# Optimization experiments

Hardware: AMD Instinct MI355X
Metric: run time of the kernel (lower is better)

Reference implementation:

```python
import jax, jax.numpy as jnp
import numpy as np
import math

B, L, IN_DIM, OUT_DIM = 2, 2048, 128, 128
H, DH = 8, 32            # num_heads, dim_head
ED = H * DH * 2          # embed_dim = 512
DEPTH = 1
LAMBDA_INIT = 0.8 - 0.6 * math.exp(-0.3 * (DEPTH + 1))
EPS = 1e-8


def setup_inputs() -> dict:
    key = jax.random.key(0)
    ks = jax.random.split(key, 10)
    x = jax.random.normal(ks[0], (B, 1, L, IN_DIM), dtype=jnp.float32)
    mask_2d = jax.random.bernoulli(ks[1], 0.9, (B, L, L))
    Wq = jax.random.normal(ks[2], (IN_DIM, ED), dtype=jnp.float32) * 0.05
    Wkv = jax.random.normal(ks[3], (IN_DIM, 2 * ED), dtype=jnp.float32) * 0.05
    Wout = jax.random.normal(ks[4], (ED, OUT_DIM), dtype=jnp.float32) * 0.05
    lambda_q1 = jax.random.normal(ks[5], (DH,), dtype=jnp.float32) * 0.1
    lambda_k1 = jax.random.normal(ks[6], (DH,), dtype=jnp.float32) * 0.1
    lambda_q2 = jax.random.normal(ks[7], (DH,), dtype=jnp.float32) * 0.1
    lambda_k2 = jax.random.normal(ks[8], (DH,), dtype=jnp.float32) * 0.1
    gamma = jnp.ones((2 * DH,), dtype=jnp.float32)
    return {"x": x, "mask_2d": mask_2d, "Wq": Wq, "Wkv": Wkv, "Wout": Wout,
            "lambda_q1": lambda_q1, "lambda_k1": lambda_k1,
            "lambda_q2": lambda_q2, "lambda_k2": lambda_k2, "gamma": gamma}


def reference(x, mask_2d, Wq, Wkv, Wout, lambda_q1, lambda_k1, lambda_q2, lambda_k2, gamma):
    b = x.shape[0]
    xs = x[:, 0]                                   # [b, L, in_dim]
    q = xs @ Wq                                    # [b, L, 2*H*DH]
    k, v = jnp.split(xs @ Wkv, 2, axis=-1)
    q = q.reshape(b, L, 2 * H, DH).transpose(0, 2, 1, 3) * (DH ** -0.5)  # [b,2H,L,d]
    k = k.reshape(b, L, 2 * H, DH).transpose(0, 2, 1, 3)                 # [b,2H,L,d]
    v = v.reshape(b, L, H, 2 * DH).transpose(0, 2, 1, 3)                 # [b,H,L,2d]
    dots = jnp.einsum('bnld,bnmd->bnlm', q, k)     # [b,2H,L,L]
    mask_value = -jnp.finfo(dots.dtype).max
    dots = jnp.where(mask_2d[:, None, :, :], dots, mask_value)
    attn_w = jax.nn.softmax(dots.astype(jnp.float32), axis=-1).astype(dots.dtype)
    lam1 = jnp.exp(jnp.sum(lambda_q1 * lambda_k1))
    lam2 = jnp.exp(jnp.sum(lambda_q2 * lambda_k2))
    lam = lam1 - lam2 + LAMBDA_INIT
    attn_w = attn_w.reshape(b, H, 2, L, L)
    attn_w = attn_w[:, :, 0] - lam * attn_w[:, :, 1]   # [b,H,L,L]
    attn = jnp.einsum('bhlm,bhmd->bhld', attn_w, v)    # [b,H,L,2d]
    rms = jnp.sqrt(jnp.mean(attn ** 2, axis=-1, keepdims=True))
    attn = gamma * (attn / (rms + EPS)) * (1.0 - LAMBDA_INIT)
    out = attn.transpose(0, 2, 1, 3).reshape(b, L, H * 2 * DH) @ Wout  # [b,L,out_dim]
    return out[:, None]                             # [b,1,L,out_dim]
```

## Files before the change

### kernel.cpp

```cpp
#include <hip/hip_runtime.h>
#include <float.h>
#include <math.h>

typedef __attribute__((ext_vector_type(8))) short short8;
typedef __attribute__((ext_vector_type(4))) float f32x4;
typedef __attribute__((ext_vector_type(4))) unsigned short ushort4v;

constexpr int SEQL = 2048;
constexpr int NQH  = 16;
constexpr int NVH  = 8;
constexpr int DHD  = 32;
constexpr float LAMB_INIT = 0.4707130183436648f;
constexpr float REPS      = 1e-8f;
constexpr float QW        = 0.25503492f;

#if __has_builtin(__builtin_amdgcn_exp2f)
#define EXPW(x) __builtin_amdgcn_exp2f(x)
#else
#define EXPW(x) exp2f(x)
#endif

static __device__ __forceinline__ unsigned short f2bf(float f) {
    union { float f; unsigned u; } a; a.f = f;
    unsigned u = a.u;
    u += 0x7fffu + ((u >> 16) & 1u);
    return (unsigned short)(u >> 16);
}

static __device__ __forceinline__ unsigned cvtpk(float lo, float hi) {
    unsigned r;
    asm("v_cvt_pk_bf16_f32 %0, %1, %2" : "=v"(r) : "v"(lo), "v"(hi));
    return r;
}

static __device__ __forceinline__ void stage16(const unsigned short* g, unsigned short* l) {
    __builtin_amdgcn_global_load_lds(
        (const __attribute__((address_space(1))) unsigned int*)g,
        (__attribute__((address_space(3))) unsigned int*)l, 16, 0, 0);
}

__global__ __launch_bounds__(256) void pack_prep_kernel(
        const unsigned char* __restrict__ mb, const int* __restrict__ mi,
        unsigned long long* __restrict__ bits,
        const float* __restrict__ x, const float* __restrict__ Wq,
        const float* __restrict__ Wkv, const float* __restrict__ Wout,
        unsigned short* __restrict__ xb, unsigned short* __restrict__ Wf,
        unsigned short* __restrict__ WfO) {
    __shared__ int cnt[256];
    int t = threadIdx.x;
    int c = 0;
    #pragma unroll
    for (int i = 0; i < 16; ++i) c += (mb[t * 16 + i] != 0);
    cnt[t] = c;
    __syncthreads();
    for (int s = 128; s > 0; s >>= 1) { if (t < s) cnt[t] += cnt[t + s]; __syncthreads(); }
    int f = cnt[0] > 2048;
    int gtid = blockIdx.x * 256 + t;
    int nthr = gridDim.x * 256;
    {
        const int total = 2 * SEQL * (SEQL / 64);
        int wid = blockIdx.x * 4 + (t >> 6);
        int lane = t & 63;
        int stride = gridDim.x * 4;
        for (int w = wid; w < total; w += stride) {
            int e = w * 64 + lane;
            int v = f ? (int)mb[e] : mi[e];
            unsigned long long b = __ballot(v != 0);
            if (lane == 0) bits[w] = b;
        }
    }
    {
        float4 v = ((const float4*)x)[gtid];
        ushort4v o = { f2bf(v.x), f2bf(v.y), f2bf(v.z), f2bf(v.w) };
        ((ushort4v*)xb)[gtid] = o;
    }
    for (int e = gtid; e < 262144; e += nthr) {
        int k = e >> 11, cc = e & 2047;
        if (cc < 1536) {
            float v = (cc < 512) ? Wq[(size_t)k * 512 + cc] * QW
                                 : Wkv[(size_t)k * 1024 + (cc - 512)];
            int cp = cc >> 4, lr = cc & 15, kk = k >> 5, lg = (k >> 3) & 3, j = k & 7;
            Wf[(((size_t)(cp * 4 + kk) * 4 + lg) * 16 + lr) * 8 + j] = f2bf(v);
        }
    }
    if (gtid < 65536) {
        int k = gtid >> 7, cc = gtid & 127;
        float v = Wout[gtid];
        int cp = cc >> 4, lr = cc & 15, kk = k >> 5, lg = (k >> 3) & 3, j = k & 7;
        WfO[(((size_t)(cp * 16 + kk) * 4 + lg) * 16 + lr) * 8 + j] = f2bf(v);
    }
}

__global__ __launch_bounds__(256) void qkv_mfma_kernel(
        const unsigned short* __restrict__ xb, const unsigned short* __restrict__ Wf,
        unsigned short* __restrict__ Q, unsigned short* __restrict__ Kf,
        unsigned short* __restrict__ Vf) {
    int t = threadIdx.x, w = t >> 6, lane = t & 63, lr = lane & 15, lg = lane >> 4;
    int lid = blockIdx.x;
    int swz = (lid & 7) * 192 + (lid >> 3);
    int by = swz >> 6, bx = swz & 63;
    int r0 = bx * 64 + w * 16;
    short8 ax[4];
    #pragma unroll
    for (int kk = 0; kk < 4; ++kk)
        ax[kk] = *(const short8*)(xb + (size_t)(r0 + lr) * 128 + kk * 32 + lg * 8);
    f32x4 acc[4];
    #pragma unroll
    for (int ct = 0; ct < 4; ++ct) acc[ct] = (f32x4){0.f, 0.f, 0.f, 0.f};
    #pragma unroll
    for (int ct = 0; ct < 4; ++ct) {
        int cp = by * 4 + ct;
        #pragma unroll
        for (int kk = 0; kk < 4; ++kk) {
            short8 bw = *(const short8*)(Wf + (size_t)(cp * 4 + kk) * 512 + lane * 8);
            acc[ct] = __builtin_amdgcn_mfma_f32_16x16x32_bf16(ax[kk], bw, acc[ct], 0, 0, 0);
        }
    }
    int gr0 = r0 + 4 * lg;
    int b = gr0 >> 11;
    if (by < 8) {
        #pragma unroll
        for (int ct = 0; ct < 4; ++ct) {
            int col = by * 64 + 16 * ct + lr;
            int n = col >> 5, d = col & 31;
            #pragma unroll
            for (int r = 0; r < 4; ++r) {
                int l = (gr0 + r) & 2047;
                Q[(((size_t)(b * NQH + n)) * SEQL + l) * DHD + d] = f2bf(acc[ct][r]);
            }
        }
    } else if (by < 16) {
        #pragma unroll
        for (int ct = 0; ct < 4; ++ct) {
            int ck = by * 64 + 16 * ct + lr - 512;
            int n = ck >> 5, dk = ck & 31;
            size_t hb = ((size_t)(b * NQH + n)) * 65536 + (dk >> 3) * 128 + (dk & 7);
            #pragma unroll
            for (int r = 0; r < 4; ++r) {
                int l = (gr0 + r) & 2047;
                Kf[hb + (size_t)((l >> 6) * 4 + ((l >> 4) & 3)) * 512 + (l & 15) * 8]
                    = f2bf(acc[ct][r]);
            }
        }
    } else {
        #pragma unroll
        for (int ct = 0; ct < 4; ++ct) {
            int cv = by * 64 + 16 * ct + lr - 1024;
            int h = cv >> 6, d = cv & 63;
            size_t hb = ((size_t)(b * NVH + h)) * 131072 + (d >> 4) * 512 + (d & 15) * 8;
            #pragma unroll
            for (int r = 0; r < 4; ++r) {
                int l = (gr0 + r) & 2047;
                Vf[hb + (size_t)((l >> 6) * 2 + ((l >> 5) & 1)) * 2048
                      + ((l >> 4) & 1) * 4 + ((l >> 2) & 3) * 128 + (l & 3)]
                    = f2bf(acc[ct][r]);
            }
        }
    }
}

__global__ __launch_bounds__(256, 2) void attn_kernel(
        const unsigned short* __restrict__ Q, const unsigned short* __restrict__ Kf,
        const unsigned short* __restrict__ Vf, const unsigned long long* __restrict__ bits,
        const float* __restrict__ lq1, const float* __restrict__ lk1,
        const float* __restrict__ lq2, const float* __restrict__ lk2,
        const float* __restrict__ gamma, unsigned short* __restrict__ A) {
    __shared__ unsigned short lds[4][8192];
    int tid = threadIdx.x;
    int w = tid >> 6, lane = tid & 63;
    int lr = lane & 15, lg = lane >> 4;
    int lid = blockIdx.y * 32 + blockIdx.x;
    int swz = (lid & 7) * 64 + (lid >> 3);
    int qtile = swz & 31, bh = swz >> 5;
    int b = bh >> 3, h = bh & 7;
    int q0 = qtile * 64 + w * 16;
    int bnA = b * NQH + 2 * h;

    short8 aqA = *(const short8*)(Q + (((size_t)bnA) * SEQL + q0 + lr) * DHD + lg * 8);
    short8 aqB = *(const short8*)(Q + (((size_t)(bnA + 1)) * SEQL + q0 + lr) * DHD + lg * 8);
    const unsigned short* KA = Kf + ((size_t)bnA) * 65536;
    const unsigned short* KB = KA + 65536;
    const unsigned short* VB = Vf + ((size_t)(b * NVH + h)) * 131072;
    const unsigned long long* mrow = bits + ((size_t)b * SEQL + q0 + lr) * 32;

    auto stage_tile = [&](int bf, int it) {
        #pragma unroll
        for (int j = 0; j < 4; ++j) {
            int c = 4 * w + j;
            const unsigned short* src =
                (c < 4) ? (KA + it * 2048 + c * 512)
              : (c < 8) ? (KB + it * 2048 + (c - 4) * 512)
                        : (VB + it * 4096 + (c - 8) * 512);
            stage16(src + lane * 8, &lds[bf][c * 512]);
        }
    };

    f32x4 oA[4], oB[4];
    #pragma unroll
    for (int m = 0; m < 4; ++m) { oA[m] = (f32x4){0,0,0,0}; oB[m] = (f32x4){0,0,0,0}; }
    float ssA = 0.f, ssB = 0.f;
    unsigned long long mw = mrow[0];

    short8 paE[4], paO[4], bvE[8], bvO[8];
    #pragma unroll
    for (int i = 0; i < 4; ++i) { paE[i] = (short8){0,0,0,0,0,0,0,0}; paO[i] = (short8){0,0,0,0,0,0,0,0}; }
    #pragma unroll
    for (int i = 0; i < 8; ++i) { bvE[i] = (short8){0,0,0,0,0,0,0,0}; bvO[i] = (short8){0,0,0,0,0,0,0,0}; }

    stage_tile(0, 0);
    stage_tile(1, 1);

    auto body = [&](int t, short8* pa, short8* pbv, short8* npa, short8* nbv) {
        unsigned long long mwc = mw;
        mw = mrow[(t + 1) & 31];
        stage_tile((t + 2) & 3, (t + 2) & 31);
        asm volatile("s_waitcnt vmcnt(10)" ::: "memory");
        __builtin_amdgcn_s_barrier();
        __builtin_amdgcn_sched_barrier(0);
        const unsigned short* L = &lds[t & 3][0];
        short8 bkA[4], bkB[4];
        #pragma unroll
        for (int c = 0; c < 4; ++c) bkA[c] = *(const short8*)(L + c * 512 + lane * 8);
        #pragma unroll
        for (int c = 0; c < 4; ++c) bkB[c] = *(const short8*)(L + 2048 + c * 512 + lane * 8);
        #pragma unroll
        for (int z = 0; z < 8; ++z) nbv[z] = *(const short8*)(L + 4096 + z * 512 + lane * 8);
        f32x4 sA[4], sB[4];
        __builtin_amdgcn_s_setprio(1);
        #pragma unroll
        for (int c = 0; c < 4; ++c)
            sA[c] = __builtin_amdgcn_mfma_f32_16x16x32_bf16(bkA[c], aqA, (f32x4){0,0,0,0}, 0, 0, 0);
        #pragma unroll
        for (int c = 0; c < 4; ++c)
            sB[c] = __builtin_amdgcn_mfma_f32_16x16x32_bf16(bkB[c], aqB, (f32x4){0,0,0,0}, 0, 0, 0);
        #pragma unroll
        for (int m = 0; m < 4; ++m) {
            oA[m] = __builtin_amdgcn_mfma_f32_16x16x32_bf16(pa[0], pbv[m], oA[m], 0, 0, 0);
            oB[m] = __builtin_amdgcn_mfma_f32_16x16x32_bf16(pa[2], pbv[m], oB[m], 0, 0, 0);
        }
        #pragma unroll
        for (int m = 0; m < 4; ++m) {
            oA[m] = __builtin_amdgcn_mfma_f32_16x16x32_bf16(pa[1], pbv[4 + m], oA[m], 0, 0, 0);
            oB[m] = __builtin_amdgcn_mfma_f32_16x16x32_bf16(pa[3], pbv[4 + m], oB[m], 0, 0, 0);
        }
        __builtin_amdgcn_s_setprio(0);
        unsigned long long mwl = mwc >> (4 * lg);
        unsigned mlo = (unsigned)mwl, mhi = (unsigned)(mwl >> 32);
        float pA[4][4], pB[4][4];
        #pragma unroll
        for (int c = 0; c < 4; ++c) {
            unsigned wv = (c < 2) ? mlo : mhi;
            int sh = (c & 1) * 16;
            #pragma unroll
            for (int r = 0; r < 4; ++r) {
                unsigned keep = (wv >> (sh + r)) & 1u;
                float eA = EXPW(sA[c][r]);
                float eB = EXPW(sB[c][r]);
                pA[c][r] = keep ? eA : 0.f;
                pB[c][r] = keep ? eB : 0.f;
            }
        }
        float acA = 0.f, acB = 0.f;
        #pragma unroll
        for (int c = 0; c < 4; ++c)
            #pragma unroll
            for (int r = 0; r < 4; ++r) { acA += pA[c][r]; acB += pB[c][r]; }
        ssA += acA; ssB += acB;
        union { short8 v; unsigned u[4]; } a0, a1, b0, b1;
        a0.u[0] = cvtpk(pA[0][0], pA[0][1]); a0.u[1] = cvtpk(pA[0][2], pA[0][3]);
        a0.u[2] = cvtpk(pA[1][0], pA[1][1]); a0.u[3] = cvtpk(pA[1][2], pA[1][3]);
        a1.u[0] = cvtpk(pA[2][0], pA[2][1]); a1.u[1] = cvtpk(pA[2][2], pA[2][3]);
        a1.u[2] = cvtpk(pA[3][0], pA[3][1]); a1.u[3] = cvtpk(pA[3][2], pA[3][3]);
        b0.u[0] = cvtpk(pB[0][0], pB[0][1]); b0.u[1] = cvtpk(pB[0][2], pB[0][3]);
        b0.u[2] = cvtpk(pB[1][0], pB[1][1]); b0.u[3] = cvtpk(pB[1][2], pB[1][3]);
        b1.u[0] = cvtpk(pB[2][0], pB[2][1]); b1.u[1] = cvtpk(pB[2][2], pB[2][3]);
        b1.u[2] = cvtpk(pB[3][0], pB[3][1]); b1.u[3] = cvtpk(pB[3][2], pB[3][3]);
        npa[0] = a0.v; npa[1] = a1.v; npa[2] = b0.v; npa[3] = b1.v;
    };

    for (int tp = 0; tp < 16; ++tp) {
        body(2 * tp,     paE, bvE, paO, bvO);
        body(2 * tp + 1, paO, bvO, paE, bvE);
    }
    #pragma unroll
    for (int m = 0; m < 4; ++m) {
        oA[m] = __builtin_amdgcn_mfma_f32_16x16x32_bf16(paE[0], bvE[m], oA[m], 0, 0, 0);
        oB[m] = __builtin_amdgcn_mfma_f32_16x16x32_bf16(paE[2], bvE[m], oB[m], 0, 0, 0);
    }
    #pragma unroll
    for (int m = 0; m < 4; ++m) {
        oA[m] = __builtin_amdgcn_mfma_f32_16x16x32_bf16(paE[1], bvE[4 + m], oA[m], 0, 0, 0);
        oB[m] = __builtin_amdgcn_mfma_f32_16x16x32_bf16(paE[3], bvE[4 + m], oB[m], 0, 0, 0);
    }
    ssA += __shfl_xor(ssA, 16, 64); ssA += __shfl_xor(ssA, 32, 64);
    ssB += __shfl_xor(ssB, 16, 64); ssB += __shfl_xor(ssB, 32, 64);
    float invA = 1.f / ssA, invB = 1.f / ssB;
    float iA[4], iB[4];
    #pragma unroll
    for (int r = 0; r < 4; ++r) {
        iA[r] = __shfl(invA, 4 * lg + r, 64);
        iB[r] = __shfl(invB, 4 * lg + r, 64);
    }
    int l31 = lane & 31;
    float t1 = lq1[l31] * lk1[l31];
    float t2 = lq2[l31] * lk2[l31];
    #pragma unroll
    for (int o = 1; o < 32; o <<= 1) { t1 += __shfl_xor(t1, o, 64); t2 += __shfl_xor(t2, o, 64); }
    float lam = __expf(t1) - __expf(t2) + LAMB_INIT;
    float dv[4][4];
    float sq[4] = {0.f, 0.f, 0.f, 0.f};
    #pragma unroll
    for (int m = 0; m < 4; ++m)
        #pragma unroll
        for (int r = 0; r < 4; ++r) {
            float v = oA[m][r] * iA[r] - lam * (oB[m][r] * iB[r]);
            dv[m][r] = v;
            sq[r] += v * v;
        }
    #pragma unroll
    for (int r = 0; r < 4; ++r) {
        #pragma unroll
        for (int o = 1; o < 16; o <<= 1) sq[r] += __shfl_xor(sq[r], o, 64);
        sq[r] = (1.f - LAMB_INIT) / (sqrtf(sq[r] * (1.f / 64.f)) + REPS);
    }
    float gm[4];
    #pragma unroll
    for (int m = 0; m < 4; ++m) gm[m] = gamma[16 * m + lr];
    unsigned short* Ab = A + ((size_t)(b * SEQL + q0 + 4 * lg)) * 512 + h * 64 + lr;
    #pragma unroll
    for (int m = 0; m < 4; ++m)
        #pragma unroll
        for (int r = 0; r < 4; ++r)
            Ab[(size_t)r * 512 + 16 * m] = f2bf(dv[m][r] * sq[r] * gm[m]);
}

__global__ __launch_bounds__(64) void proj_mfma_kernel(
        const unsigned short* __restrict__ Ab, const unsigned short* __restrict__ WfO,
        float* __restrict__ out) {
    int lane = threadIdx.x & 63, lr = lane & 15, lg = lane >> 4;
    int r0 = blockIdx.x * 16;
    f32x4 acc[8];
    #pragma unroll
    for (int ct = 0; ct < 8; ++ct) acc[ct] = (f32x4){0.f, 0.f, 0.f, 0.f};
    #pragma unroll
    for (int kk = 0; kk < 16; ++kk) {
        short8 af = *(const short8*)(Ab + (size_t)(r0 + lr) * 512 + kk * 32 + lg * 8);
        #pragma unroll
        for (int ct = 0; ct < 8; ++ct) {
            short8 bf = *(const short8*)(WfO + (size_t)(ct * 16 + kk) * 512 + lane * 8);
            acc[ct] = __builtin_amdgcn_mfma_f32_16x16x32_bf16(af, bf, acc[ct], 0, 0, 0);
        }
    }
    #pragma unroll
    for (int ct = 0; ct < 8; ++ct)
        #pragma unroll
        for (int r = 0; r < 4; ++r)
            out[(size_t)(r0 + 4 * lg + r) * 128 + ct * 16 + lr] = acc[ct][r];
}

extern "C" void kernel_launch(void* const* d_in, const int* in_sizes, int n_in,
                              void* d_out, int out_size, void* d_ws, size_t ws_size,
                              hipStream_t stream) {
    const float* x    = (const float*)d_in[0];
    const void*  mask = d_in[1];
    const float* Wq   = (const float*)d_in[2];
    const float* Wkv  = (const float*)d_in[3];
    const float* Wout = (const float*)d_in[4];
    const float* lq1  = (const float*)d_in[5];
    const float* lk1  = (const float*)d_in[6];
    const float* lq2  = (const float*)d_in[7];
    const float* lk2  = (const float*)d_in[8];
    const float* gam  = (const float*)d_in[9];
    float* out = (float*)d_out;

    char* wsb = (char*)d_ws;
    unsigned long long* bits = (unsigned long long*)(wsb + 4096);
    unsigned short* Q        = (unsigned short*)(wsb + 1052672);
    unsigned short* Kf       = (unsigned short*)(wsb + 5246976);
    unsigned short* Vf       = (unsigned short*)(wsb + 9441280);
    unsigned short* xb       = (unsigned short*)(wsb + 13635584);
    unsigned short* Wf       = (unsigned short*)(wsb + 14684160);
    unsigned short* WfO      = (unsigned short*)(wsb + 15077376);
    unsigned short* Ab       = (unsigned short*)(wsb + 15208448);

    pack_prep_kernel<<<512, 256, 0, stream>>>((const unsigned char*)mask,
                                              (const int*)mask, bits,
                                              x, Wq, Wkv, Wout, xb, Wf, WfO);
    qkv_mfma_kernel<<<1536, 256, 0, stream>>>(xb, Wf, Q, Kf, Vf);
    attn_kernel<<<dim3(32, 16), 256, 0, stream>>>(Q, Kf, Vf, bits,
                                                  lq1, lk1, lq2, lk2, gam, Ab);
    proj_mfma_kernel<<<256, 64, 0, stream>>>(Ab, WfO, out);
}
```

Baseline: 93.89 us.

## Split attention key range across two wave halves with LDS reduction

The attention kernel now runs 512 threads per block. The two halves of the block each process half of the key sequence using 32-key tiles, with their own staging buffers. The partial outputs and row sums are reduced through LDS at the end, and the exp is switched to a raw v_exp_f32 asm. This raises the number of waves in flight per query tile to hide latency better. The cost is an extra reduction pass through shared memory and smaller per-iteration MFMA batches.

```diff
diff --git a/kernel.cpp b/kernel.cpp
--- a/kernel.cpp
+++ b/kernel.cpp
@@ -14,12 +14,6 @@
 constexpr float REPS      = 1e-8f;
 constexpr float QW        = 0.25503492f;
 
-#if __has_builtin(__builtin_amdgcn_exp2f)
-#define EXPW(x) __builtin_amdgcn_exp2f(x)
-#else
-#define EXPW(x) exp2f(x)
-#endif
-
 static __device__ __forceinline__ unsigned short f2bf(float f) {
     union { float f; unsigned u; } a; a.f = f;
     unsigned u = a.u;
@@ -30,6 +24,12 @@
 static __device__ __forceinline__ unsigned cvtpk(float lo, float hi) {
     unsigned r;
     asm("v_cvt_pk_bf16_f32 %0, %1, %2" : "=v"(r) : "v"(lo), "v"(hi));
+    return r;
+}
+
+static __device__ __forceinline__ float expv(float x) {
+    float r;
+    asm("v_exp_f32 %0, %1" : "=v"(r) : "v"(x));
     return r;
 }
 
@@ -159,138 +159,156 @@
     }
 }
 
-__global__ __launch_bounds__(256, 2) void attn_kernel(
+__global__ __launch_bounds__(512, 4) void attn_kernel(
         const unsigned short* __restrict__ Q, const unsigned short* __restrict__ Kf,
         const unsigned short* __restrict__ Vf, const unsigned long long* __restrict__ bits,
         const float* __restrict__ lq1, const float* __restrict__ lk1,
         const float* __restrict__ lq2, const float* __restrict__ lk2,
         const float* __restrict__ gamma, unsigned short* __restrict__ A) {
-    __shared__ unsigned short lds[4][8192];
+    __shared__ unsigned short lds[2][4][4096];
     int tid = threadIdx.x;
     int w = tid >> 6, lane = tid & 63;
     int lr = lane & 15, lg = lane >> 4;
+    int half = w >> 2, ws = w & 3;
     int lid = blockIdx.y * 32 + blockIdx.x;
     int swz = (lid & 7) * 64 + (lid >> 3);
     int qtile = swz & 31, bh = swz >> 5;
     int b = bh >> 3, h = bh & 7;
-    int q0 = qtile * 64 + w * 16;
+    int q0 = qtile * 64 + ws * 16;
     int bnA = b * NQH + 2 * h;
+    int kb = half * 1024;
 
     short8 aqA = *(const short8*)(Q + (((size_t)bnA) * SEQL + q0 + lr) * DHD + lg * 8);
     short8 aqB = *(const short8*)(Q + (((size_t)(bnA + 1)) * SEQL + q0 + lr) * DHD + lg * 8);
-    const unsigned short* KA = Kf + ((size_t)bnA) * 65536;
-    const unsigned short* KB = KA + 65536;
-    const unsigned short* VB = Vf + ((size_t)(b * NVH + h)) * 131072;
-    const unsigned long long* mrow = bits + ((size_t)b * SEQL + q0 + lr) * 32;
-
-    auto stage_tile = [&](int bf, int it) {
-        #pragma unroll
-        for (int j = 0; j < 4; ++j) {
-            int c = 4 * w + j;
-            const unsigned short* src =
-                (c < 4) ? (KA + it * 2048 + c * 512)
-              : (c < 8) ? (KB + it * 2048 + (c - 4) * 512)
-                        : (VB + it * 4096 + (c - 8) * 512);
-            stage16(src + lane * 8, &lds[bf][c * 512]);
-        }
+    const unsigned short* KA = Kf + ((size_t)bnA) * 65536 + kb * 32;
+    const unsigned short* KB = Kf + ((size_t)(bnA + 1)) * 65536 + kb * 32;
+    const unsigned short* VB = Vf + ((size_t)(b * NVH + h)) * 131072 + (size_t)kb * 64;
+    const unsigned* mrow = (const unsigned*)bits + ((size_t)b * SEQL + q0 + lr) * 64 + kb / 32;
+
+    const unsigned short* gsrc;
+    int gstride;
+    if (ws == 0)      { gsrc = KA;        gstride = 1024; }
+    else if (ws == 1) { gsrc = KB;        gstride = 1024; }
+    else if (ws == 2) { gsrc = VB;        gstride = 2048; }
+    else              { gsrc = VB + 1024; gstride = 2048; }
+    const unsigned short* gl = gsrc + lane * 8;
+    unsigned ldso = ws * 1024;
+    unsigned short* lbase = &lds[half][0][0];
+
+    auto stage2 = [&](int bf, int it) {
+        stage16(gl + (size_t)it * gstride,       lbase + bf * 4096 + ldso);
+        stage16(gl + (size_t)it * gstride + 512, lbase + bf * 4096 + ldso + 512);
     };
 
     f32x4 oA[4], oB[4];
     #pragma unroll
     for (int m = 0; m < 4; ++m) { oA[m] = (f32x4){0,0,0,0}; oB[m] = (f32x4){0,0,0,0}; }
     float ssA = 0.f, ssB = 0.f;
-    unsigned long long mw = mrow[0];
-
-    short8 paE[4], paO[4], bvE[8], bvO[8];
-    #pragma unroll
-    for (int i = 0; i < 4; ++i) { paE[i] = (short8){0,0,0,0,0,0,0,0}; paO[i] = (short8){0,0,0,0,0,0,0,0}; }
-    #pragma unroll
-    for (int i = 0; i < 8; ++i) { bvE[i] = (short8){0,0,0,0,0,0,0,0}; bvO[i] = (short8){0,0,0,0,0,0,0,0}; }
-
-    stage_tile(0, 0);
-    stage_tile(1, 1);
-
-    auto body = [&](int t, short8* pa, short8* pbv, short8* npa, short8* nbv) {
-        unsigned long long mwc = mw;
-        mw = mrow[(t + 1) & 31];
-        stage_tile((t + 2) & 3, (t + 2) & 31);
-        asm volatile("s_waitcnt vmcnt(10)" ::: "memory");
-        __builtin_amdgcn_s_barrier();
-        __builtin_amdgcn_sched_barrier(0);
-        const unsigned short* L = &lds[t & 3][0];
-        short8 bkA[4], bkB[4];
-        #pragma unroll
-        for (int c = 0; c < 4; ++c) bkA[c] = *(const short8*)(L + c * 512 + lane * 8);
-        #pragma unroll
-        for (int c = 0; c < 4; ++c) bkB[c] = *(const short8*)(L + 2048 + c * 512 + lane * 8);
-        #pragma unroll
-        for (int z = 0; z < 8; ++z) nbv[z] = *(const short8*)(L + 4096 + z * 512 + lane * 8);
-        f32x4 sA[4], sB[4];
-        __builtin_amdgcn_s_setprio(1);
-        #pragma unroll
-        for (int c = 0; c < 4; ++c)
-            sA[c] = __builtin_amdgcn_mfma_f32_16x16x32_bf16(bkA[c], aqA, (f32x4){0,0,0,0}, 0, 0, 0);
-        #pragma unroll
-        for (int c = 0; c < 4; ++c)
-            sB[c] = __builtin_amdgcn_mfma_f32_16x16x32_bf16(bkB[c], aqB, (f32x4){0,0,0,0}, 0, 0, 0);
+    const f32x4 Z = {0.f, 0.f, 0.f, 0.f};
+    short8 paA[2], paB[2];
+    paA[0] = paA[1] = paB[0] = paB[1] = (short8){0,0,0,0,0,0,0,0};
+
+    stage2(0, 0);
+    stage2(1, 1);
+    *(short8*)(lbase + 3 * 4096 + 2048 + ws * 512 + lane * 8) = (short8){0,0,0,0,0,0,0,0};
+    unsigned mw = mrow[0];
+    __syncthreads();
+
+    for (int tt = 0; tt < 32; tt += 4) {
+        #pragma unroll
+        for (int u = 0; u < 4; ++u) {
+            const int t_ = tt + u;
+            asm volatile("s_waitcnt vmcnt(3)" ::: "memory");
+            __builtin_amdgcn_s_barrier();
+            __builtin_amdgcn_sched_barrier(0);
+            stage2((u + 2) & 3, (t_ + 2) & 31);
+            unsigned mwc = mw;
+            mw = mrow[(t_ + 1) & 31];
+            const unsigned short* L  = lbase + u * 4096;
+            const unsigned short* Lp = lbase + ((u + 3) & 3) * 4096 + 2048;
+            short8 bkA[2], bkB[2], bv[4];
+            bkA[0] = *(const short8*)(L + lane * 8);
+            bkA[1] = *(const short8*)(L + 512 + lane * 8);
+            bkB[0] = *(const short8*)(L + 1024 + lane * 8);
+            bkB[1] = *(const short8*)(L + 1536 + lane * 8);
+            #pragma unroll
+            for (int m = 0; m < 4; ++m) bv[m] = *(const short8*)(Lp + m * 512 + lane * 8);
+            f32x4 sA[2], sB[2];
+            __builtin_amdgcn_s_setprio(1);
+            sA[0] = __builtin_amdgcn_mfma_f32_16x16x32_bf16(bkA[0], aqA, Z, 0, 0, 0);
+            sA[1] = __builtin_amdgcn_mfma_f32_16x16x32_bf16(bkA[1], aqA, Z, 0, 0, 0);
+            sB[0] = __builtin_amdgcn_mfma_f32_16x16x32_bf16(bkB[0], aqB, Z, 0, 0, 0);
+            sB[1] = __builtin_amdgcn_mfma_f32_16x16x32_bf16(bkB[1], aqB, Z, 0, 0, 0);
+            const int pp = (u & 1) ^ 1;
+            #pragma unroll
+            for (int m = 0; m < 4; ++m) {
+                oA[m] = __builtin_amdgcn_mfma_f32_16x16x32_bf16(paA[pp], bv[m], oA[m], 0, 0, 0);
+                oB[m] = __builtin_amdgcn_mfma_f32_16x16x32_bf16(paB[pp], bv[m], oB[m], 0, 0, 0);
+            }
+            __builtin_amdgcn_s_setprio(0);
+            unsigned wv = mwc >> (4 * lg);
+            float pAv[2][4], pBv[2][4];
+            #pragma unroll
+            for (int c = 0; c < 2; ++c)
+                #pragma unroll
+                for (int r = 0; r < 4; ++r) {
+                    unsigned keep = (wv >> (16 * c + r)) & 1u;
+                    float eA = expv(sA[c][r]);
+                    float eB = expv(sB[c][r]);
+                    pAv[c][r] = keep ? eA : 0.f;
+                    pBv[c][r] = keep ? eB : 0.f;
+                }
+            ssA += ((pAv[0][0] + pAv[0][1]) + (pAv[0][2] + pAv[0][3]))
+                 + ((pAv[1][0] + pAv[1][1]) + (pAv[1][2] + pAv[1][3]));
+            ssB += ((pBv[0][0] + pBv[0][1]) + (pBv[0][2] + pBv[0][3]))
+                 + ((pBv[1][0] + pBv[1][1]) + (pBv[1][2] + pBv[1][3]));
+            union { short8 v; unsigned uu[4]; } xa, xb2;
+            xa.uu[0]  = cvtpk(pAv[0][0], pAv[0][1]); xa.uu[1]  = cvtpk(pAv[0][2], pAv[0][3]);
+            xa.uu[2]  = cvtpk(pAv[1][0], pAv[1][1]); xa.uu[3]  = cvtpk(pAv[1][2], pAv[1][3]);
+            xb2.uu[0] = cvtpk(pBv[0][0], pBv[0][1]); xb2.uu[1] = cvtpk(pBv[0][2], pBv[0][3]);
+            xb2.uu[2] = cvtpk(pBv[1][0], pBv[1][1]); xb2.uu[3] = cvtpk(pBv[1][2], pBv[1][3]);
+            paA[u & 1] = xa.v; paB[u & 1] = xb2.v;
+        }
+    }
+    {
+        const unsigned short* Lp = lbase + 3 * 4096 + 2048;
+        short8 bv[4];
+        #pragma unroll
+        for (int m = 0; m < 4; ++m) bv[m] = *(const short8*)(Lp + m * 512 + lane * 8);
         #pragma unroll
         for (int m = 0; m < 4; ++m) {
-            oA[m] = __builtin_amdgcn_mfma_f32_16x16x32_bf16(pa[0], pbv[m], oA[m], 0, 0, 0);
-            oB[m] = __builtin_amdgcn_mfma_f32_16x16x32_bf16(pa[2], pbv[m], oB[m], 0, 0, 0);
-        }
-        #pragma unroll
-        for (int m = 0; m < 4; ++m) {
-            oA[m] = __builtin_amdgcn_mfma_f32_16x16x32_bf16(pa[1], pbv[4 + m], oA[m], 0, 0, 0);
-            oB[m] = __builtin_amdgcn_mfma_f32_16x16x32_bf16(pa[3], pbv[4 + m], oB[m], 0, 0, 0);
-        }
-        __builtin_amdgcn_s_setprio(0);
-        unsigned long long mwl = mwc >> (4 * lg);
-        unsigned mlo = (unsigned)mwl, mhi = (unsigned)(mwl >> 32);
-        float pA[4][4], pB[4][4];
-        #pragma unroll
-        for (int c = 0; c < 4; ++c) {
-            unsigned wv = (c < 2) ? mlo : mhi;
-            int sh = (c & 1) * 16;
+            oA[m] = __builtin_amdgcn_mfma_f32_16x16x32_bf16(paA[1], bv[m], oA[m], 0, 0, 0);
+            oB[m] = __builtin_amdgcn_mfma_f32_16x16x32_bf16(paB[1], bv[m], oB[m], 0, 0, 0);
+        }
+    }
+    asm volatile("s_waitcnt vmcnt(0)" ::: "memory");
+    __syncthreads();
+    float* fb = (float*)&lds[0][0][0];
+    if (half) {
+        int rg = ws * 2048;
+        #pragma unroll
+        for (int m = 0; m < 4; ++m)
             #pragma unroll
             for (int r = 0; r < 4; ++r) {
-                unsigned keep = (wv >> (sh + r)) & 1u;
-                float eA = EXPW(sA[c][r]);
-                float eB = EXPW(sB[c][r]);
-                pA[c][r] = keep ? eA : 0.f;
-                pB[c][r] = keep ? eB : 0.f;
-            }
-        }
-        float acA = 0.f, acB = 0.f;
-        #pragma unroll
-        for (int c = 0; c < 4; ++c)
-            #pragma unroll
-            for (int r = 0; r < 4; ++r) { acA += pA[c][r]; acB += pB[c][r]; }
-        ssA += acA; ssB += acB;
-        union { short8 v; unsigned u[4]; } a0, a1, b0, b1;
-        a0.u[0] = cvtpk(pA[0][0], pA[0][1]); a0.u[1] = cvtpk(pA[0][2], pA[0][3]);
-        a0.u[2] = cvtpk(pA[1][0], pA[1][1]); a0.u[3] = cvtpk(pA[1][2], pA[1][3]);
-        a1.u[0] = cvtpk(pA[2][0], pA[2][1]); a1.u[1] = cvtpk(pA[2][2], pA[2][3]);
-        a1.u[2] = cvtpk(pA[3][0], pA[3][1]); a1.u[3] = cvtpk(pA[3][2], pA[3][3]);
-        b0.u[0] = cvtpk(pB[0][0], pB[0][1]); b0.u[1] = cvtpk(pB[0][2], pB[0][3]);
-        b0.u[2] = cvtpk(pB[1][0], pB[1][1]); b0.u[3] = cvtpk(pB[1][2], pB[1][3]);
-        b1.u[0] = cvtpk(pB[2][0], pB[2][1]); b1.u[1] = cvtpk(pB[2][2], pB[2][3]);
-        b1.u[2] = cvtpk(pB[3][0], pB[3][1]); b1.u[3] = cvtpk(pB[3][2], pB[3][3]);
-        npa[0] = a0.v; npa[1] = a1.v; npa[2] = b0.v; npa[3] = b1.v;
-    };
-
-    for (int tp = 0; tp < 16; ++tp) {
-        body(2 * tp,     paE, bvE, paO, bvO);
-        body(2 * tp + 1, paO, bvO, paE, bvE);
-    }
-    #pragma unroll
-    for (int m = 0; m < 4; ++m) {
-        oA[m] = __builtin_amdgcn_mfma_f32_16x16x32_bf16(paE[0], bvE[m], oA[m], 0, 0, 0);
-        oB[m] = __builtin_amdgcn_mfma_f32_16x16x32_bf16(paE[2], bvE[m], oB[m], 0, 0, 0);
-    }
-    #pragma unroll
-    for (int m = 0; m < 4; ++m) {
-        oA[m] = __builtin_amdgcn_mfma_f32_16x16x32_bf16(paE[1], bvE[4 + m], oA[m], 0, 0, 0);
-        oB[m] = __builtin_amdgcn_mfma_f32_16x16x32_bf16(paE[3], bvE[4 + m], oB[m], 0, 0, 0);
+                fb[rg + (m * 4 + r) * 64 + lane]        = oA[m][r];
+                fb[rg + (16 + m * 4 + r) * 64 + lane]   = oB[m][r];
+            }
+        fb[8192 + ws * 128 + 2 * lane]     = ssA;
+        fb[8192 + ws * 128 + 2 * lane + 1] = ssB;
+    }
+    __syncthreads();
+    if (half) return;
+    {
+        int rg = ws * 2048;
+        #pragma unroll
+        for (int m = 0; m < 4; ++m)
+            #pragma unroll
+            for (int r = 0; r < 4; ++r) {
+                oA[m][r] += fb[rg + (m * 4 + r) * 64 + lane];
+                oB[m][r] += fb[rg + (16 + m * 4 + r) * 64 + lane];
+            }
+        ssA += fb[8192 + ws * 128 + 2 * lane];
+        ssB += fb[8192 + ws * 128 + 2 * lane + 1];
     }
     ssA += __shfl_xor(ssA, 16, 64); ssA += __shfl_xor(ssA, 32, 64);
     ssB += __shfl_xor(ssB, 16, 64); ssB += __shfl_xor(ssB, 32, 64);
@@ -387,7 +405,7 @@
                                               (const int*)mask, bits,
                                               x, Wq, Wkv, Wout, xb, Wf, WfO);
     qkv_mfma_kernel<<<1536, 256, 0, stream>>>(xb, Wf, Q, Kf, Vf);
-    attn_kernel<<<dim3(32, 16), 256, 0, stream>>>(Q, Kf, Vf, bits,
+    attn_kernel<<<dim3(32, 16), 512, 0, stream>>>(Q, Kf, Vf, bits,
                                                   lq1, lk1, lq2, lk2, gam, Ab);
     proj_mfma_kernel<<<256, 64, 0, stream>>>(Ab, WfO, out);
 }
```

New measurement: 108.6 us. 1.16x slower.

## Split differential attention per query head and add separate merge kernel

Applied to the files above, without the earlier changes.

The attention kernel now processes one query head per block instead of the paired heads, doubling the grid to 1024 blocks with a 3-stage LDS ring instead of 4 and launch bounds raised to 4 blocks per CU. The software-pipelined P@V overlap across iterations is dropped for a simpler in-iteration schedule. The lambda subtraction, RMS normalisation and gamma scaling move to a new merge kernel that reads bf16 per-head outputs from a new workspace buffer. This aims at more parallelism and occupancy. The cost is an extra launch, V tiles loaded twice (once per head of the pair), an extra global round trip for the intermediate output, and bf16 rounding before the head subtraction.

```diff
diff --git a/kernel.cpp b/kernel.cpp
--- a/kernel.cpp
+++ b/kernel.cpp
@@ -14,12 +14,6 @@
 constexpr float REPS      = 1e-8f;
 constexpr float QW        = 0.25503492f;
 
-#if __has_builtin(__builtin_amdgcn_exp2f)
-#define EXPW(x) __builtin_amdgcn_exp2f(x)
-#else
-#define EXPW(x) exp2f(x)
-#endif
-
 static __device__ __forceinline__ unsigned short f2bf(float f) {
     union { float f; unsigned u; } a; a.f = f;
     unsigned u = a.u;
@@ -27,9 +21,20 @@
     return (unsigned short)(u >> 16);
 }
 
+static __device__ __forceinline__ float bf2f(unsigned short s) {
+    union { unsigned u; float f; } a; a.u = ((unsigned)s) << 16;
+    return a.f;
+}
+
 static __device__ __forceinline__ unsigned cvtpk(float lo, float hi) {
     unsigned r;
     asm("v_cvt_pk_bf16_f32 %0, %1, %2" : "=v"(r) : "v"(lo), "v"(hi));
+    return r;
+}
+
+static __device__ __forceinline__ float expv(float x) {
+    float r;
+    asm("v_exp_f32 %0, %1" : "=v"(r) : "v"(x));
     return r;
 }
 
@@ -159,94 +164,69 @@
     }
 }
 
-__global__ __launch_bounds__(256, 2) void attn_kernel(
+__global__ __launch_bounds__(256, 4) void attn_kernel(
         const unsigned short* __restrict__ Q, const unsigned short* __restrict__ Kf,
         const unsigned short* __restrict__ Vf, const unsigned long long* __restrict__ bits,
-        const float* __restrict__ lq1, const float* __restrict__ lk1,
-        const float* __restrict__ lq2, const float* __restrict__ lk2,
-        const float* __restrict__ gamma, unsigned short* __restrict__ A) {
-    __shared__ unsigned short lds[4][8192];
+        unsigned short* __restrict__ O) {
+    __shared__ unsigned short lds[3][6144];
     int tid = threadIdx.x;
     int w = tid >> 6, lane = tid & 63;
     int lr = lane & 15, lg = lane >> 4;
     int lid = blockIdx.y * 32 + blockIdx.x;
-    int swz = (lid & 7) * 64 + (lid >> 3);
-    int qtile = swz & 31, bh = swz >> 5;
-    int b = bh >> 3, h = bh & 7;
+    int swz = (lid & 7) * 128 + (lid >> 3);
+    int qtile = swz & 31, bn = swz >> 5;
+    int b = bn >> 4, n = bn & 15, vh = n >> 1;
     int q0 = qtile * 64 + w * 16;
-    int bnA = b * NQH + 2 * h;
-
-    short8 aqA = *(const short8*)(Q + (((size_t)bnA) * SEQL + q0 + lr) * DHD + lg * 8);
-    short8 aqB = *(const short8*)(Q + (((size_t)(bnA + 1)) * SEQL + q0 + lr) * DHD + lg * 8);
-    const unsigned short* KA = Kf + ((size_t)bnA) * 65536;
-    const unsigned short* KB = KA + 65536;
-    const unsigned short* VB = Vf + ((size_t)(b * NVH + h)) * 131072;
+
+    short8 aq = *(const short8*)(Q + (((size_t)bn) * SEQL + q0 + lr) * DHD + lg * 8);
+    const unsigned short* KH = Kf + ((size_t)bn) * 65536;
+    const unsigned short* VH = Vf + ((size_t)(b * NVH + vh)) * 131072;
     const unsigned long long* mrow = bits + ((size_t)b * SEQL + q0 + lr) * 32;
 
     auto stage_tile = [&](int bf, int it) {
         #pragma unroll
-        for (int j = 0; j < 4; ++j) {
-            int c = 4 * w + j;
-            const unsigned short* src =
-                (c < 4) ? (KA + it * 2048 + c * 512)
-              : (c < 8) ? (KB + it * 2048 + (c - 4) * 512)
-                        : (VB + it * 4096 + (c - 8) * 512);
+        for (int j = 0; j < 3; ++j) {
+            int c = 3 * w + j;
+            const unsigned short* src = (c < 4)
+                ? (KH + (size_t)it * 2048 + c * 512)
+                : (VH + (size_t)it * 4096 + (c - 4) * 512);
             stage16(src + lane * 8, &lds[bf][c * 512]);
         }
     };
 
-    f32x4 oA[4], oB[4];
-    #pragma unroll
-    for (int m = 0; m < 4; ++m) { oA[m] = (f32x4){0,0,0,0}; oB[m] = (f32x4){0,0,0,0}; }
-    float ssA = 0.f, ssB = 0.f;
-    unsigned long long mw = mrow[0];
-
-    short8 paE[4], paO[4], bvE[8], bvO[8];
-    #pragma unroll
-    for (int i = 0; i < 4; ++i) { paE[i] = (short8){0,0,0,0,0,0,0,0}; paO[i] = (short8){0,0,0,0,0,0,0,0}; }
-    #pragma unroll
-    for (int i = 0; i < 8; ++i) { bvE[i] = (short8){0,0,0,0,0,0,0,0}; bvO[i] = (short8){0,0,0,0,0,0,0,0}; }
+    f32x4 oacc[4];
+    #pragma unroll
+    for (int m = 0; m < 4; ++m) oacc[m] = (f32x4){0.f, 0.f, 0.f, 0.f};
+    float ssum = 0.f;
+    const f32x4 Z = {0.f, 0.f, 0.f, 0.f};
 
     stage_tile(0, 0);
     stage_tile(1, 1);
-
-    auto body = [&](int t, short8* pa, short8* pbv, short8* npa, short8* nbv) {
+    unsigned long long mw = mrow[0];
+
+    for (int t = 0; t < 32; ++t) {
+        asm volatile("s_waitcnt vmcnt(4)" ::: "memory");
+        __builtin_amdgcn_s_barrier();
+        __builtin_amdgcn_sched_barrier(0);
+        stage_tile((t + 2) % 3, (t + 2) & 31);
         unsigned long long mwc = mw;
         mw = mrow[(t + 1) & 31];
-        stage_tile((t + 2) & 3, (t + 2) & 31);
-        asm volatile("s_waitcnt vmcnt(10)" ::: "memory");
-        __builtin_amdgcn_s_barrier();
         __builtin_amdgcn_sched_barrier(0);
-        const unsigned short* L = &lds[t & 3][0];
-        short8 bkA[4], bkB[4];
-        #pragma unroll
-        for (int c = 0; c < 4; ++c) bkA[c] = *(const short8*)(L + c * 512 + lane * 8);
-        #pragma unroll
-        for (int c = 0; c < 4; ++c) bkB[c] = *(const short8*)(L + 2048 + c * 512 + lane * 8);
-        #pragma unroll
-        for (int z = 0; z < 8; ++z) nbv[z] = *(const short8*)(L + 4096 + z * 512 + lane * 8);
-        f32x4 sA[4], sB[4];
+        const unsigned short* L = &lds[t % 3][0];
+        short8 bk[4], bv[8];
+        #pragma unroll
+        for (int c = 0; c < 4; ++c) bk[c] = *(const short8*)(L + c * 512 + lane * 8);
+        #pragma unroll
+        for (int z = 0; z < 8; ++z) bv[z] = *(const short8*)(L + 2048 + z * 512 + lane * 8);
+        f32x4 s[4];
         __builtin_amdgcn_s_setprio(1);
         #pragma unroll
         for (int c = 0; c < 4; ++c)
-            sA[c] = __builtin_amdgcn_mfma_f32_16x16x32_bf16(bkA[c], aqA, (f32x4){0,0,0,0}, 0, 0, 0);
-        #pragma unroll
-        for (int c = 0; c < 4; ++c)
-            sB[c] = __builtin_amdgcn_mfma_f32_16x16x32_bf16(bkB[c], aqB, (f32x4){0,0,0,0}, 0, 0, 0);
-        #pragma unroll
-        for (int m = 0; m < 4; ++m) {
-            oA[m] = __builtin_amdgcn_mfma_f32_16x16x32_bf16(pa[0], pbv[m], oA[m], 0, 0, 0);
-            oB[m] = __builtin_amdgcn_mfma_f32_16x16x32_bf16(pa[2], pbv[m], oB[m], 0, 0, 0);
-        }
-        #pragma unroll
-        for (int m = 0; m < 4; ++m) {
-            oA[m] = __builtin_amdgcn_mfma_f32_16x16x32_bf16(pa[1], pbv[4 + m], oA[m], 0, 0, 0);
-            oB[m] = __builtin_amdgcn_mfma_f32_16x16x32_bf16(pa[3], pbv[4 + m], oB[m], 0, 0, 0);
-        }
+            s[c] = __builtin_amdgcn_mfma_f32_16x16x32_bf16(bk[c], aq, Z, 0, 0, 0);
         __builtin_amdgcn_s_setprio(0);
         unsigned long long mwl = mwc >> (4 * lg);
         unsigned mlo = (unsigned)mwl, mhi = (unsigned)(mwl >> 32);
-        float pA[4][4], pB[4][4];
+        float p[4][4];
         #pragma unroll
         for (int c = 0; c < 4; ++c) {
             unsigned wv = (c < 2) ? mlo : mhi;
@@ -254,84 +234,84 @@
             #pragma unroll
             for (int r = 0; r < 4; ++r) {
                 unsigned keep = (wv >> (sh + r)) & 1u;
-                float eA = EXPW(sA[c][r]);
-                float eB = EXPW(sB[c][r]);
-                pA[c][r] = keep ? eA : 0.f;
-                pB[c][r] = keep ? eB : 0.f;
+                float e = expv(s[c][r]);
+                p[c][r] = keep ? e : 0.f;
             }
         }
-        float acA = 0.f, acB = 0.f;
+        float ac = 0.f;
         #pragma unroll
         for (int c = 0; c < 4; ++c)
             #pragma unroll
-            for (int r = 0; r < 4; ++r) { acA += pA[c][r]; acB += pB[c][r]; }
-        ssA += acA; ssB += acB;
-        union { short8 v; unsigned u[4]; } a0, a1, b0, b1;
-        a0.u[0] = cvtpk(pA[0][0], pA[0][1]); a0.u[1] = cvtpk(pA[0][2], pA[0][3]);
-        a0.u[2] = cvtpk(pA[1][0], pA[1][1]); a0.u[3] = cvtpk(pA[1][2], pA[1][3]);
-        a1.u[0] = cvtpk(pA[2][0], pA[2][1]); a1.u[1] = cvtpk(pA[2][2], pA[2][3]);
-        a1.u[2] = cvtpk(pA[3][0], pA[3][1]); a1.u[3] = cvtpk(pA[3][2], pA[3][3]);
-        b0.u[0] = cvtpk(pB[0][0], pB[0][1]); b0.u[1] = cvtpk(pB[0][2], pB[0][3]);
-        b0.u[2] = cvtpk(pB[1][0], pB[1][1]); b0.u[3] = cvtpk(pB[1][2], pB[1][3]);
-        b1.u[0] = cvtpk(pB[2][0], pB[2][1]); b1.u[1] = cvtpk(pB[2][2], pB[2][3]);
-        b1.u[2] = cvtpk(pB[3][0], pB[3][1]); b1.u[3] = cvtpk(pB[3][2], pB[3][3]);
-        npa[0] = a0.v; npa[1] = a1.v; npa[2] = b0.v; npa[3] = b1.v;
-    };
-
-    for (int tp = 0; tp < 16; ++tp) {
-        body(2 * tp,     paE, bvE, paO, bvO);
-        body(2 * tp + 1, paO, bvO, paE, bvE);
-    }
-    #pragma unroll
-    for (int m = 0; m < 4; ++m) {
-        oA[m] = __builtin_amdgcn_mfma_f32_16x16x32_bf16(paE[0], bvE[m], oA[m], 0, 0, 0);
-        oB[m] = __builtin_amdgcn_mfma_f32_16x16x32_bf16(paE[2], bvE[m], oB[m], 0, 0, 0);
-    }
-    #pragma unroll
-    for (int m = 0; m < 4; ++m) {
-        oA[m] = __builtin_amdgcn_mfma_f32_16x16x32_bf16(paE[1], bvE[4 + m], oA[m], 0, 0, 0);
-        oB[m] = __builtin_amdgcn_mfma_f32_16x16x32_bf16(paE[3], bvE[4 + m], oB[m], 0, 0, 0);
-    }
-    ssA += __shfl_xor(ssA, 16, 64); ssA += __shfl_xor(ssA, 32, 64);
-    ssB += __shfl_xor(ssB, 16, 64); ssB += __shfl_xor(ssB, 32, 64);
-    float invA = 1.f / ssA, invB = 1.f / ssB;
-    float iA[4], iB[4];
-    #pragma unroll
-    for (int r = 0; r < 4; ++r) {
-        iA[r] = __shfl(invA, 4 * lg + r, 64);
-        iB[r] = __shfl(invB, 4 * lg + r, 64);
-    }
-    int l31 = lane & 31;
+            for (int r = 0; r < 4; ++r) ac += p[c][r];
+        ssum += ac;
+        union { short8 v; unsigned u[4]; } a0, a1;
+        a0.u[0] = cvtpk(p[0][0], p[0][1]); a0.u[1] = cvtpk(p[0][2], p[0][3]);
+        a0.u[2] = cvtpk(p[1][0], p[1][1]); a0.u[3] = cvtpk(p[1][2], p[1][3]);
+        a1.u[0] = cvtpk(p[2][0], p[2][1]); a1.u[1] = cvtpk(p[2][2], p[2][3]);
+        a1.u[2] = cvtpk(p[3][0], p[3][1]); a1.u[3] = cvtpk(p[3][2], p[3][3]);
+        __builtin_amdgcn_s_setprio(1);
+        #pragma unroll
+        for (int m = 0; m < 4; ++m)
+            oacc[m] = __builtin_amdgcn_mfma_f32_16x16x32_bf16(a0.v, bv[m], oacc[m], 0, 0, 0);
+        #pragma unroll
+        for (int m = 0; m < 4; ++m)
+            oacc[m] = __builtin_amdgcn_mfma_f32_16x16x32_bf16(a1.v, bv[4 + m], oacc[m], 0, 0, 0);
+        __builtin_amdgcn_s_setprio(0);
+    }
+    asm volatile("s_waitcnt vmcnt(0)" ::: "memory");
+    ssum += __shfl_xor(ssum, 16, 64);
+    ssum += __shfl_xor(ssum, 32, 64);
+    float inv = 1.f / ssum;
+    float invr[4];
+    #pragma unroll
+    for (int r = 0; r < 4; ++r) invr[r] = __shfl(inv, 4 * lg + r, 64);
+    unsigned short* Ob = O + (((size_t)bn) * SEQL + q0 + 4 * lg) * 64 + lr;
+    #pragma unroll
+    for (int m = 0; m < 4; ++m)
+        #pragma unroll
+        for (int r = 0; r < 4; ++r)
+            Ob[(size_t)r * 64 + 16 * m] = f2bf(oacc[m][r] * invr[r]);
+}
+
+__global__ __launch_bounds__(256) void merge_kernel(
+        const unsigned short* __restrict__ O,
+        const float* __restrict__ lq1, const float* __restrict__ lk1,
+        const float* __restrict__ lq2, const float* __restrict__ lk2,
+        const float* __restrict__ gamma, unsigned short* __restrict__ Ab) {
+    int t = threadIdx.x;
+    int T = blockIdx.x * 256 + t;
+    int row = T >> 2, part = T & 3;
+    int b = row >> 14, h = (row >> 11) & 7, l = row & 2047;
+    int l31 = t & 31;
     float t1 = lq1[l31] * lk1[l31];
     float t2 = lq2[l31] * lk2[l31];
     #pragma unroll
     for (int o = 1; o < 32; o <<= 1) { t1 += __shfl_xor(t1, o, 64); t2 += __shfl_xor(t2, o, 64); }
     float lam = __expf(t1) - __expf(t2) + LAMB_INIT;
-    float dv[4][4];
-    float sq[4] = {0.f, 0.f, 0.f, 0.f};
-    #pragma unroll
-    for (int m = 0; m < 4; ++m)
-        #pragma unroll
-        for (int r = 0; r < 4; ++r) {
-            float v = oA[m][r] * iA[r] - lam * (oB[m][r] * iB[r]);
-            dv[m][r] = v;
-            sq[r] += v * v;
-        }
-    #pragma unroll
-    for (int r = 0; r < 4; ++r) {
-        #pragma unroll
-        for (int o = 1; o < 16; o <<= 1) sq[r] += __shfl_xor(sq[r], o, 64);
-        sq[r] = (1.f - LAMB_INIT) / (sqrtf(sq[r] * (1.f / 64.f)) + REPS);
-    }
-    float gm[4];
-    #pragma unroll
-    for (int m = 0; m < 4; ++m) gm[m] = gamma[16 * m + lr];
-    unsigned short* Ab = A + ((size_t)(b * SEQL + q0 + 4 * lg)) * 512 + h * 64 + lr;
-    #pragma unroll
-    for (int m = 0; m < 4; ++m)
-        #pragma unroll
-        for (int r = 0; r < 4; ++r)
-            Ab[(size_t)r * 512 + 16 * m] = f2bf(dv[m][r] * sq[r] * gm[m]);
+    const unsigned short* p1 = O + (((size_t)(b * NQH + 2 * h)) * SEQL + l) * 64 + part * 16;
+    const unsigned short* p2 = p1 + (size_t)SEQL * 64;
+    short8 a0 = *(const short8*)p1, a1 = *(const short8*)(p1 + 8);
+    short8 b0 = *(const short8*)p2, b1 = *(const short8*)(p2 + 8);
+    float v[16]; float sq = 0.f;
+    #pragma unroll
+    for (int i = 0; i < 8; ++i) {
+        v[i]     = bf2f((unsigned short)a0[i]) - lam * bf2f((unsigned short)b0[i]);
+        v[8 + i] = bf2f((unsigned short)a1[i]) - lam * bf2f((unsigned short)b1[i]);
+    }
+    #pragma unroll
+    for (int i = 0; i < 16; ++i) sq += v[i] * v[i];
+    sq += __shfl_xor(sq, 1, 64);
+    sq += __shfl_xor(sq, 2, 64);
+    float sc = (1.f - LAMB_INIT) / (sqrtf(sq * (1.f / 64.f)) + REPS);
+    unsigned short* dst = Ab + ((size_t)(b * SEQL + l)) * 512 + h * 64 + part * 16;
+    short8 o0, o1;
+    #pragma unroll
+    for (int i = 0; i < 8; ++i) {
+        o0[i] = (short)f2bf(v[i]     * sc * gamma[part * 16 + i]);
+        o1[i] = (short)f2bf(v[8 + i] * sc * gamma[part * 16 + 8 + i]);
+    }
+    *(short8*)dst = o0;
+    *(short8*)(dst + 8) = o1;
 }
 
 __global__ __launch_bounds__(64) void proj_mfma_kernel(
@@ -382,12 +362,13 @@
     unsigned short* Wf       = (unsigned short*)(wsb + 14684160);
     unsigned short* WfO      = (unsigned short*)(wsb + 15077376);
     unsigned short* Ab       = (unsigned short*)(wsb + 15208448);
+    unsigned short* O        = (unsigned short*)(wsb + 19402752);
 
     pack_prep_kernel<<<512, 256, 0, stream>>>((const unsigned char*)mask,
                                               (const int*)mask, bits,
                                               x, Wq, Wkv, Wout, xb, Wf, WfO);
     qkv_mfma_kernel<<<1536, 256, 0, stream>>>(xb, Wf, Q, Kf, Vf);
-    attn_kernel<<<dim3(32, 16), 256, 0, stream>>>(Q, Kf, Vf, bits,
-                                                  lq1, lk1, lq2, lk2, gam, Ab);
+    attn_kernel<<<dim3(32, 32), 256, 0, stream>>>(Q, Kf, Vf, bits, O);
+    merge_kernel<<<512, 256, 0, stream>>>(O, lq1, lk1, lq2, lk2, gam, Ab);
     proj_mfma_kernel<<<256, 64, 0, stream>>>(Ab, WfO, out);
 }
```

After: 100.2 us. +6.8%, slower.
